# Optimization experiments

Hardware: AMD Instinct MI355X
Metric: run time of the kernel (lower is better)

## Reference

```python
import jax, jax.numpy as jnp
import numpy as np

NUM_FIELDS = 50
CARD = 10000  # per-field cardinality; global index = x + field_offset
FACTOR_DIM = 64
ATT_SIZE = 64
BATCH = 2048


def setup_inputs() -> dict:
    key = jax.random.key(0)
    ks = jax.random.split(key, 5)
    x = jax.random.randint(ks[0], (BATCH, NUM_FIELDS), 0, CARD, dtype=jnp.int64)
    emb = jax.random.normal(ks[1], (NUM_FIELDS * CARD, FACTOR_DIM), jnp.float32) * 0.1
    W1 = jax.random.normal(ks[2], (FACTOR_DIM, ATT_SIZE), jnp.float32) * 0.1
    b1 = jnp.zeros((ATT_SIZE,), jnp.float32)
    w2 = jax.random.normal(ks[3], (ATT_SIZE, 1), jnp.float32) * 0.1
    b2 = jnp.zeros((1,), jnp.float32)
    lin_w = jax.random.normal(ks[4], (NUM_FIELDS * CARD, 1), jnp.float32) * 0.1
    lin_b = jnp.zeros((1,), jnp.float32)
    return {"x": x, "emb": emb, "W1": W1, "b1": b1, "w2": w2, "b2": b2,
            "lin_w": lin_w, "lin_b": lin_b}


def reference(x, emb, W1, b1, w2, b2, lin_w, lin_b):
    F = NUM_FIELDS
    offsets = (jnp.arange(F, dtype=x.dtype) * CARD)[None, :]  # [1, F]
    idx = x + offsets                                          # [B, F] global ids
    factors = emb[idx]                                         # [B, F, D]
    iu, ju = np.triu_indices(F, k=1)                           # P = F*(F-1)/2 pairs (i < j)
    inter = factors[:, iu, :] * factors[:, ju, :]              # [B, P, D]
    # attention MLP: Dense -> ReLU -> Dense(1) -> Softmax over pair axis
    h = jax.nn.relu(jnp.einsum('bpd,da->bpa', inter, W1) + b1)
    logits = jnp.einsum('bpa,ao->bpo', h, w2) + b2             # [B, P, 1]
    scores = jax.nn.softmax(logits, axis=1)
    inter_sum = jnp.sum(inter, axis=-1, keepdims=True)         # [B, P, 1]
    attended = jnp.sum(inter_sum * scores, axis=1)             # [B, 1]
    linear = jnp.sum(lin_w[idx], axis=1) + lin_b               # [B, 1]
    return linear + attended
```

## Files before the change

### kernel.cpp

```cpp
#include <hip/hip_runtime.h>
#include <hip/hip_bf16.h>

#define NF 50
#define NCARD 10000
#define FD 64
#define NPAIR 1225
#define NPAIR_PAD 1232
#define NTILE 77
#define FSH 72

typedef _Float16 h16x8 __attribute__((ext_vector_type(8)));
typedef float f32x4 __attribute__((ext_vector_type(4)));

__global__ __launch_bounds__(256) void afm_kernel(
    const int* __restrict__ x,
    const float* __restrict__ emb,
    const float* __restrict__ W1,
    const float* __restrict__ b1,
    const float* __restrict__ w2,
    const float* __restrict__ lin_w,
    const float* __restrict__ lin_b,
    float* __restrict__ out)
{
    __shared__ __align__(16) _Float16 fach[NF * FSH];
    __shared__ float plog[NPAIR_PAD];
    __shared__ float pis[NPAIR_PAD];
    __shared__ unsigned poff[NPAIR_PAD];
    __shared__ float s_red[8];
    __shared__ float s_red2[8];
    __shared__ float s_linear;

    const int b    = blockIdx.x;
    const int tid  = threadIdx.x;
    const int lane = tid & 63;
    const int wid  = tid >> 6;
    const int n16  = lane & 15;
    const int quad = lane >> 4;

    if (tid == 0) s_linear = 0.f;
    __syncthreads();

    const int* xrow = x + b * NF;
    for (int t = tid; t < NF * 8; t += 256) {
        int f = t >> 3, q = t & 7;
        int gid = xrow[f] + f * NCARD;
        const float* src = emb + (size_t)gid * FD + q * 8;
        float4 v0 = *(const float4*)(src);
        float4 v1 = *(const float4*)(src + 4);
        h16x8 h;
        h[0] = (_Float16)v0.x; h[1] = (_Float16)v0.y;
        h[2] = (_Float16)v0.z; h[3] = (_Float16)v0.w;
        h[4] = (_Float16)v1.x; h[5] = (_Float16)v1.y;
        h[6] = (_Float16)v1.z; h[7] = (_Float16)v1.w;
        *(h16x8*)(fach + f * FSH + q * 8) = h;
    }
    if (tid < NF) {
        int gid = xrow[tid] + tid * NCARD;
        atomicAdd(&s_linear, lin_w[gid]);
    }
    for (int p = tid; p < NPAIR_PAD; p += 256) {
        int i = 0, j = 0;
        if (p < NPAIR) {
            float disc = (float)((2 * NF - 1) * (2 * NF - 1) - 8 * p);
            i = (int)(((float)(2 * NF - 1) - sqrtf(disc)) * 0.5f);
            if (i < 0) i = 0;
            if (i > NF - 2) i = NF - 2;
            while (i + 1 <= NF - 2 && (i + 1) * (NF - 1) - ((i + 1) * i) / 2 <= p) ++i;
            while (i > 0 && i * (NF - 1) - (i * (i - 1)) / 2 > p) --i;
            j = p - (i * (NF - 1) - (i * (i - 1)) / 2) + i + 1;
        }
        poff[p] = (unsigned)(i * (FSH * 2)) | ((unsigned)(j * (FSH * 2)) << 16);
    }

    h16x8 afragW[4][2];
    #pragma unroll
    for (int mt = 0; mt < 4; ++mt) {
        int a = mt * 16 + n16;
        #pragma unroll
        for (int ks = 0; ks < 2; ++ks) {
            h16x8 av;
            #pragma unroll
            for (int jj = 0; jj < 8; ++jj) {
                int k = ks * 32 + quad * 8 + jj;
                av[jj] = (_Float16)W1[k * 64 + a];
            }
            afragW[mt][ks] = av;
        }
    }
    h16x8 aones;
    {
        _Float16 o = (n16 == 0) ? (_Float16)1.0f : (_Float16)0.0f;
        #pragma unroll
        for (int jj = 0; jj < 8; ++jj) aones[jj] = o;
    }
    f32x4 b1v[4], w2v[4];
    #pragma unroll
    for (int mt = 0; mt < 4; ++mt) {
        const float4 bb = *(const float4*)(b1 + mt * 16 + quad * 4);
        const float4 ww = *(const float4*)(w2 + mt * 16 + quad * 4);
        b1v[mt] = (f32x4){bb.x, bb.y, bb.z, bb.w};
        w2v[mt] = (f32x4){ww.x, ww.y, ww.z, ww.w};
    }
    __syncthreads();

    const char* fbase = (const char*)fach;
    for (int t = wid; t < NTILE; t += 4) {
        const int p0 = t * 16;
        const unsigned po = poff[p0 + n16];
        const char* pbi = fbase + (po & 0xFFFFu) + quad * 16;
        const char* pbj = fbase + (po >> 16) + quad * 16;

        f32x4 acc[4];
        #pragma unroll
        for (int mt = 0; mt < 4; ++mt) acc[mt] = b1v[mt];
        f32x4 accS = {0.f, 0.f, 0.f, 0.f};

        #pragma unroll
        for (int ks = 0; ks < 2; ++ks) {
            h16x8 fi = *(const h16x8*)(pbi + ks * 64);
            h16x8 fj = *(const h16x8*)(pbj + ks * 64);
            h16x8 pr = fi * fj;
            #pragma unroll
            for (int mt = 0; mt < 4; ++mt)
                acc[mt] = __builtin_amdgcn_mfma_f32_16x16x32_f16(afragW[mt][ks], pr, acc[mt], 0, 0, 0);
            accS = __builtin_amdgcn_mfma_f32_16x16x32_f16(aones, pr, accS, 0, 0, 0);
        }

        float lacc = 0.f;
        #pragma unroll
        for (int mt = 0; mt < 4; ++mt) {
            #pragma unroll
            for (int r = 0; r < 4; ++r)
                lacc += fmaxf(acc[mt][r], 0.f) * w2v[mt][r];
        }
        lacc += __shfl_xor(lacc, 16, 64);
        lacc += __shfl_xor(lacc, 32, 64);
        if (lane < 16) {
            plog[p0 + lane] = lacc;
            pis[p0 + lane] = accS[0];
        }
    }
    __syncthreads();

    float mx = -1e30f;
    for (int p = tid; p < NPAIR; p += 256) mx = fmaxf(mx, plog[p]);
    #pragma unroll
    for (int m = 32; m >= 1; m >>= 1) mx = fmaxf(mx, __shfl_xor(mx, m, 64));
    if (lane == 0) s_red[wid] = mx;
    __syncthreads();
    mx = fmaxf(fmaxf(s_red[0], s_red[1]), fmaxf(s_red[2], s_red[3]));
    __syncthreads();

    float se = 0.f, sei = 0.f;
    for (int p = tid; p < NPAIR; p += 256) {
        float e = __expf(plog[p] - mx);
        se  += e;
        sei += e * pis[p];
    }
    #pragma unroll
    for (int m = 32; m >= 1; m >>= 1) {
        se  += __shfl_xor(se, m, 64);
        sei += __shfl_xor(sei, m, 64);
    }
    if (lane == 0) { s_red[wid] = se; s_red2[wid] = sei; }
    __syncthreads();
    if (tid == 0) {
        float tse  = s_red[0] + s_red[1] + s_red[2] + s_red[3];
        float tsei = s_red2[0] + s_red2[1] + s_red2[2] + s_red2[3];
        out[b] = s_linear + lin_b[0] + tsei / tse;
    }
}

extern "C" void kernel_launch(void* const* d_in, const int* in_sizes, int n_in,
                              void* d_out, int out_size, void* d_ws, size_t ws_size,
                              hipStream_t stream) {
    const int*   x     = (const int*)d_in[0];
    const float* emb   = (const float*)d_in[1];
    const float* W1    = (const float*)d_in[2];
    const float* b1    = (const float*)d_in[3];
    const float* w2    = (const float*)d_in[4];
    const float* lin_w = (const float*)d_in[6];
    const float* lin_b = (const float*)d_in[7];
    float* out = (float*)d_out;
    const int batch = out_size;
    afm_kernel<<<batch, 256, 0, stream>>>(x, emb, W1, b1, w2, lin_w, lin_b, out);
}
```

Baseline: 218.9 us.

## Precompute W1 fragments and pair offsets, fuse online softmax, two batches per block

A small pre-kernel moves the W1 fp16 fragment packing and the pair-index decoding into a one-off launch that writes to workspace. Each main block now handles two batch rows, with two waves per row. The softmax becomes an online max/sum kept in registers per tile, which removes the shared plog/pis arrays and several block-wide reductions and barriers. The linear term uses a wave shuffle reduction instead of shared atomics. In exchange there is an extra kernel launch, and with half as many blocks each row gets only two waves, which may reduce parallelism.

```diff
diff --git a/kernel.cpp b/kernel.cpp
--- a/kernel.cpp
+++ b/kernel.cpp
@@ -7,43 +7,75 @@
 #define NPAIR 1225
 #define NPAIR_PAD 1232
 #define NTILE 77
-#define FSH 72
+#define NB 2
+#define FROWB 144
+#define FBATB 7200
 
 typedef _Float16 h16x8 __attribute__((ext_vector_type(8)));
 typedef float f32x4 __attribute__((ext_vector_type(4)));
 
-__global__ __launch_bounds__(256) void afm_kernel(
+__global__ void afm_pre(const float* __restrict__ W1,
+                        _Float16* __restrict__ w1f,
+                        unsigned* __restrict__ poffg) {
+    const int bid = blockIdx.x, tid = threadIdx.x;
+    if (bid < 2) {
+        const int slot = bid * 4 + (tid >> 6);
+        const int lane = tid & 63;
+        const int n16 = lane & 15, quad = lane >> 4;
+        const int mt = slot >> 1, ks = slot & 1;
+        const int a = mt * 16 + n16;
+        h16x8 v;
+        #pragma unroll
+        for (int jj = 0; jj < 8; ++jj) {
+            int k = ks * 32 + quad * 8 + jj;
+            v[jj] = (_Float16)W1[k * 64 + a];
+        }
+        *(h16x8*)(w1f + ((size_t)(slot * 64 + lane)) * 8) = v;
+    } else {
+        int p = (bid - 2) * 256 + tid;
+        if (p < NPAIR_PAD) {
+            int i = 0, j = 0;
+            if (p < NPAIR) {
+                float disc = (float)((2 * NF - 1) * (2 * NF - 1) - 8 * p);
+                i = (int)(((float)(2 * NF - 1) - sqrtf(disc)) * 0.5f);
+                if (i < 0) i = 0;
+                if (i > NF - 2) i = NF - 2;
+                while (i + 1 <= NF - 2 && (i + 1) * (NF - 1) - ((i + 1) * i) / 2 <= p) ++i;
+                while (i > 0 && i * (NF - 1) - (i * (i - 1)) / 2 > p) --i;
+                j = p - (i * (NF - 1) - (i * (i - 1)) / 2) + i + 1;
+            }
+            poffg[p] = (unsigned)(i * FROWB) | ((unsigned)(j * FROWB) << 16);
+        }
+    }
+}
+
+__global__ __launch_bounds__(256, 4) void afm_main(
     const int* __restrict__ x,
     const float* __restrict__ emb,
-    const float* __restrict__ W1,
     const float* __restrict__ b1,
     const float* __restrict__ w2,
     const float* __restrict__ lin_w,
     const float* __restrict__ lin_b,
+    const _Float16* __restrict__ w1f,
+    const unsigned* __restrict__ poffg,
     float* __restrict__ out)
 {
-    __shared__ __align__(16) _Float16 fach[NF * FSH];
-    __shared__ float plog[NPAIR_PAD];
-    __shared__ float pis[NPAIR_PAD];
+    __shared__ __align__(16) _Float16 fach[NB * 50 * 72];
     __shared__ unsigned poff[NPAIR_PAD];
-    __shared__ float s_red[8];
-    __shared__ float s_red2[8];
-    __shared__ float s_linear;
-
-    const int b    = blockIdx.x;
+    __shared__ float cmb[4][3];
+
+    const int b0   = blockIdx.x * NB;
     const int tid  = threadIdx.x;
     const int lane = tid & 63;
     const int wid  = tid >> 6;
     const int n16  = lane & 15;
     const int quad = lane >> 4;
 
-    if (tid == 0) s_linear = 0.f;
-    __syncthreads();
-
-    const int* xrow = x + b * NF;
-    for (int t = tid; t < NF * 8; t += 256) {
-        int f = t >> 3, q = t & 7;
-        int gid = xrow[f] + f * NCARD;
+    for (int t = tid; t < NB * 50 * 8; t += 256) {
+        int rowid = t >> 3, q = t & 7;
+        int bb = (rowid >= 50) ? 1 : 0;
+        int f = rowid - bb * 50;
+        int gid = x[(b0 + bb) * NF + f] + f * NCARD;
         const float* src = emb + (size_t)gid * FD + q * 8;
         float4 v0 = *(const float4*)(src);
         float4 v1 = *(const float4*)(src + 4);
@@ -52,41 +84,14 @@
         h[2] = (_Float16)v0.z; h[3] = (_Float16)v0.w;
         h[4] = (_Float16)v1.x; h[5] = (_Float16)v1.y;
         h[6] = (_Float16)v1.z; h[7] = (_Float16)v1.w;
-        *(h16x8*)(fach + f * FSH + q * 8) = h;
-    }
-    if (tid < NF) {
-        int gid = xrow[tid] + tid * NCARD;
-        atomicAdd(&s_linear, lin_w[gid]);
-    }
-    for (int p = tid; p < NPAIR_PAD; p += 256) {
-        int i = 0, j = 0;
-        if (p < NPAIR) {
-            float disc = (float)((2 * NF - 1) * (2 * NF - 1) - 8 * p);
-            i = (int)(((float)(2 * NF - 1) - sqrtf(disc)) * 0.5f);
-            if (i < 0) i = 0;
-            if (i > NF - 2) i = NF - 2;
-            while (i + 1 <= NF - 2 && (i + 1) * (NF - 1) - ((i + 1) * i) / 2 <= p) ++i;
-            while (i > 0 && i * (NF - 1) - (i * (i - 1)) / 2 > p) --i;
-            j = p - (i * (NF - 1) - (i * (i - 1)) / 2) + i + 1;
-        }
-        poff[p] = (unsigned)(i * (FSH * 2)) | ((unsigned)(j * (FSH * 2)) << 16);
-    }
-
-    h16x8 afragW[4][2];
+        *(h16x8*)(fach + bb * 3600 + f * 72 + q * 8) = h;
+    }
+    for (int p = tid; p < NPAIR_PAD; p += 256) poff[p] = poffg[p];
+
+    h16x8 afragW[8];
     #pragma unroll
-    for (int mt = 0; mt < 4; ++mt) {
-        int a = mt * 16 + n16;
-        #pragma unroll
-        for (int ks = 0; ks < 2; ++ks) {
-            h16x8 av;
-            #pragma unroll
-            for (int jj = 0; jj < 8; ++jj) {
-                int k = ks * 32 + quad * 8 + jj;
-                av[jj] = (_Float16)W1[k * 64 + a];
-            }
-            afragW[mt][ks] = av;
-        }
-    }
+    for (int s = 0; s < 8; ++s)
+        afragW[s] = *(const h16x8*)(w1f + ((size_t)(s * 64 + lane)) * 8);
     h16x8 aones;
     {
         _Float16 o = (n16 == 0) ? (_Float16)1.0f : (_Float16)0.0f;
@@ -103,28 +108,30 @@
     }
     __syncthreads();
 
-    const char* fbase = (const char*)fach;
-    for (int t = wid; t < NTILE; t += 4) {
-        const int p0 = t * 16;
-        const unsigned po = poff[p0 + n16];
-        const char* pbi = fbase + (po & 0xFFFFu) + quad * 16;
-        const char* pbj = fbase + (po >> 16) + quad * 16;
+    const int mybatch = wid >> 1;
+    const char* fb = (const char*)fach + mybatch * FBATB;
+    float m = -1e30f, se = 0.f, sei = 0.f;
+
+    for (int t = (wid & 1); t < NTILE; t += 2) {
+        const unsigned po = poff[t * 16 + n16];
+        const char* pbi = fb + (po & 0xFFFFu) + quad * 16;
+        const char* pbj = fb + (po >> 16) + quad * 16;
+
+        h16x8 fi0 = *(const h16x8*)(pbi);
+        h16x8 fj0 = *(const h16x8*)(pbj);
+        h16x8 fi1 = *(const h16x8*)(pbi + 64);
+        h16x8 fj1 = *(const h16x8*)(pbj + 64);
+        h16x8 pr0 = fi0 * fj0;
+        h16x8 pr1 = fi1 * fj1;
 
         f32x4 acc[4];
         #pragma unroll
-        for (int mt = 0; mt < 4; ++mt) acc[mt] = b1v[mt];
-        f32x4 accS = {0.f, 0.f, 0.f, 0.f};
-
-        #pragma unroll
-        for (int ks = 0; ks < 2; ++ks) {
-            h16x8 fi = *(const h16x8*)(pbi + ks * 64);
-            h16x8 fj = *(const h16x8*)(pbj + ks * 64);
-            h16x8 pr = fi * fj;
-            #pragma unroll
-            for (int mt = 0; mt < 4; ++mt)
-                acc[mt] = __builtin_amdgcn_mfma_f32_16x16x32_f16(afragW[mt][ks], pr, acc[mt], 0, 0, 0);
-            accS = __builtin_amdgcn_mfma_f32_16x16x32_f16(aones, pr, accS, 0, 0, 0);
-        }
+        for (int mt = 0; mt < 4; ++mt) {
+            acc[mt] = __builtin_amdgcn_mfma_f32_16x16x32_f16(afragW[mt * 2 + 0], pr0, b1v[mt], 0, 0, 0);
+            acc[mt] = __builtin_amdgcn_mfma_f32_16x16x32_f16(afragW[mt * 2 + 1], pr1, acc[mt], 0, 0, 0);
+        }
+        f32x4 accS = __builtin_amdgcn_mfma_f32_16x16x32_f16(aones, pr0, (f32x4){0.f, 0.f, 0.f, 0.f}, 0, 0, 0);
+        accS = __builtin_amdgcn_mfma_f32_16x16x32_f16(aones, pr1, accS, 0, 0, 0);
 
         float lacc = 0.f;
         #pragma unroll
@@ -135,39 +142,49 @@
         }
         lacc += __shfl_xor(lacc, 16, 64);
         lacc += __shfl_xor(lacc, 32, 64);
-        if (lane < 16) {
-            plog[p0 + lane] = lacc;
-            pis[p0 + lane] = accS[0];
-        }
-    }
+        float is = __shfl(accS[0], n16, 64);
+
+        if (t * 16 + n16 >= NPAIR) lacc = -1e30f;
+
+        float nm = fmaxf(m, lacc);
+        float sc = __expf(m - nm);
+        float e  = __expf(lacc - nm);
+        se  = se * sc + e;
+        sei = sei * sc + e * is;
+        m = nm;
+    }
+
+    #pragma unroll
+    for (int d = 1; d <= 8; d <<= 1) {
+        float m2   = __shfl_xor(m, d, 64);
+        float se2  = __shfl_xor(se, d, 64);
+        float sei2 = __shfl_xor(sei, d, 64);
+        float nm = fmaxf(m, m2);
+        float a = __expf(m - nm), bsc = __expf(m2 - nm);
+        se  = se * a + se2 * bsc;
+        sei = sei * a + sei2 * bsc;
+        m = nm;
+    }
+
+    float lin = 0.f;
+    if ((wid & 1) == 0) {
+        if (lane < NF) {
+            int gid = x[(b0 + mybatch) * NF + lane] + lane * NCARD;
+            lin = lin_w[gid];
+        }
+        #pragma unroll
+        for (int d = 1; d <= 32; d <<= 1) lin += __shfl_xor(lin, d, 64);
+    }
+
+    if (lane == 0) { cmb[wid][0] = m; cmb[wid][1] = se; cmb[wid][2] = sei; }
     __syncthreads();
-
-    float mx = -1e30f;
-    for (int p = tid; p < NPAIR; p += 256) mx = fmaxf(mx, plog[p]);
-    #pragma unroll
-    for (int m = 32; m >= 1; m >>= 1) mx = fmaxf(mx, __shfl_xor(mx, m, 64));
-    if (lane == 0) s_red[wid] = mx;
-    __syncthreads();
-    mx = fmaxf(fmaxf(s_red[0], s_red[1]), fmaxf(s_red[2], s_red[3]));
-    __syncthreads();
-
-    float se = 0.f, sei = 0.f;
-    for (int p = tid; p < NPAIR; p += 256) {
-        float e = __expf(plog[p] - mx);
-        se  += e;
-        sei += e * pis[p];
-    }
-    #pragma unroll
-    for (int m = 32; m >= 1; m >>= 1) {
-        se  += __shfl_xor(se, m, 64);
-        sei += __shfl_xor(sei, m, 64);
-    }
-    if (lane == 0) { s_red[wid] = se; s_red2[wid] = sei; }
-    __syncthreads();
-    if (tid == 0) {
-        float tse  = s_red[0] + s_red[1] + s_red[2] + s_red[3];
-        float tsei = s_red2[0] + s_red2[1] + s_red2[2] + s_red2[3];
-        out[b] = s_linear + lin_b[0] + tsei / tse;
+    if ((wid & 1) == 0 && lane == 0) {
+        float m2 = cmb[wid + 1][0], se2 = cmb[wid + 1][1], sei2 = cmb[wid + 1][2];
+        float nm = fmaxf(m, m2);
+        float a = __expf(m - nm), bsc = __expf(m2 - nm);
+        float tse  = se * a + se2 * bsc;
+        float tsei = sei * a + sei2 * bsc;
+        out[b0 + mybatch] = lin + lin_b[0] + tsei / tse;
     }
 }
 
@@ -182,6 +199,11 @@
     const float* lin_w = (const float*)d_in[6];
     const float* lin_b = (const float*)d_in[7];
     float* out = (float*)d_out;
+
+    _Float16* w1f   = (_Float16*)d_ws;
+    unsigned* poffg = (unsigned*)((char*)d_ws + 8192);
+
+    afm_pre<<<7, 256, 0, stream>>>(W1, w1f, poffg);
     const int batch = out_size;
-    afm_kernel<<<batch, 256, 0, stream>>>(x, emb, W1, b1, w2, lin_w, lin_b, out);
+    afm_main<<<batch / NB, 256, 0, stream>>>(x, emb, b1, w2, lin_w, lin_b, w1f, poffg, out);
 }
```

Result: no change. 215.5 us (-1.6%).
